# Optimization experiments

Hardware: AMD Instinct MI355X
Metric: run time of the kernel (lower is better)

The kernel has to match this reference:

```python
import jax, jax.numpy as jnp
import numpy as np

N, H, M, B = 512, 64, 1024, 256
ETA = 1.0
INIT_STD = 0.01

def setup_inputs() -> dict:
    key = jax.random.key(0)
    k1, k2, k3, k4 = jax.random.split(key, 4)
    # Binary +/-1 sequences and memory (as produced upstream in the repo)
    sequences = jnp.where(jax.random.uniform(k1, (B, N)) < 0.5, -1.0, 1.0).astype(jnp.float32)
    memory = jnp.where(jax.random.uniform(k2, (M, N)) < 0.5, -1.0, 1.0).astype(jnp.float32)
    A_logits = (INIT_STD * jax.random.normal(k3, (N, H, N))).astype(jnp.float32)
    B_logits = (INIT_STD * jax.random.normal(k4, (H, N))).astype(jnp.float32)
    return {"sequences": sequences, "memory": memory, "A_logits": A_logits, "B_logits": B_logits}

def reference(sequences, memory, A_logits, B_logits):
    # Vectorized version of DAM.train_batch's loss over positions n=1..N-1.
    n_dim = sequences.shape[1]
    # Causal mask: row for position n attends to indices i < n. Rows n=1..N-1.
    ns = jnp.arange(1, n_dim)[:, None, None]            # (N-1,1,1)
    idx = jnp.arange(n_dim)[None, None, :]              # (1,1,N)
    mask = idx < ns                                      # (N-1,1,N)
    neg_inf = jnp.asarray(-jnp.inf, A_logits.dtype)
    A = jax.nn.softmax(jnp.where(mask, A_logits[1:], neg_inf), axis=-1)  # (N-1,H,N), zeros outside mask
    Bn = jax.nn.softmax(B_logits, axis=-1)               # (H,N)
    phi_mu = jnp.einsum('hn,mn->mh', Bn, memory)         # (M,H) memory keys
    hat_phi = jnp.einsum('bi,nhi->bnh', sequences, A)    # (B,N-1,H) queries for every position at once
    score = ETA * jnp.einsum('bnh,mh->bnm', hat_phi, phi_mu)  # (B,N-1,M)
    pi = jax.nn.softmax(score, axis=-1)                  # retrieval distribution over memories
    plus = (memory[:, 1:] > 0).astype(pi.dtype)          # (M,N-1): memory bit at position n is +1
    prob = jnp.einsum('bnm,mn->bn', pi, plus)            # P(next bit = +1)
    prob = jnp.clip(prob, 1e-6, 1.0 - 1e-6)
    target = (sequences[:, 1:] > 0).astype(prob.dtype)
    bce = -(target * jnp.log(prob) + (1.0 - target) * jnp.log1p(-prob))
    # mean over batch per position, summed over positions, / (N-1) == global mean
    return jnp.mean(bce)
```

## Files before the change

### kernel.cpp

```cpp
#include <hip/hip_runtime.h>
#include <stdint.h>

#define NPOS 512
#define NH   64
#define NM   1024
#define NB   256
#define NM1  511

typedef __attribute__((ext_vector_type(8)))  short bf16x8;
typedef __attribute__((ext_vector_type(16))) float f32x16;
typedef __attribute__((ext_vector_type(4)))  float f32x4;
typedef __attribute__((ext_vector_type(4)))  int   i32x4;

#if __has_builtin(__builtin_amdgcn_exp2f)
#define EXP2F(x) __builtin_amdgcn_exp2f(x)
#else
#define EXP2F(x) __expf((x) * 0.69314718055994531f)
#endif

__device__ __forceinline__ unsigned short f2bf(float x) {
    unsigned u = __float_as_uint(x);
    u = (u + 0x7FFFu + ((u >> 16) & 1u)) >> 16;
    return (unsigned short)u;
}
__device__ __forceinline__ int pack2(unsigned short a, unsigned short b) {
    return (int)a | ((int)b << 16);
}


__global__ __launch_bounds__(256, 4)
void kAE_prep(const float* __restrict__ seq, const float* __restrict__ Bl,
              const float* __restrict__ mem, const float* __restrict__ Al,
              unsigned short* __restrict__ seq_bf, float* __restrict__ BnT,
              float* __restrict__ plusT, unsigned short* __restrict__ Ew,
              float* __restrict__ Zb, float* __restrict__ out) {
    const int bid = blockIdx.x, t = threadIdx.x;
    if (bid < 128) {
        if (bid == 0 && t == 0) out[0] = 0.f;
        int idx = (bid * 256 + t) * 4;
        f32x4 v = *(const f32x4*)(seq + idx);
        int2 o;
        o.x = pack2(f2bf(v.x), f2bf(v.y));
        o.y = pack2(f2bf(v.z), f2bf(v.w));
        *(int2*)(seq_bf + idx) = o;
    } else if (bid < 144) {
        const int h = (bid - 128) * 4 + (t >> 6), l = t & 63;
        float v[8]; float mx = -1e30f;
#pragma unroll
        for (int j = 0; j < 8; j++) { v[j] = Bl[h * NPOS + l + 64 * j]; mx = fmaxf(mx, v[j]); }
#pragma unroll
        for (int o = 32; o; o >>= 1) mx = fmaxf(mx, __shfl_xor(mx, o));
        float s = 0.f;
#pragma unroll
        for (int j = 0; j < 8; j++) { v[j] = __expf(v[j] - mx); s += v[j]; }
#pragma unroll
        for (int o = 32; o; o >>= 1) s += __shfl_xor(s, o);
        float r = 1.0f / s;
#pragma unroll
        for (int j = 0; j < 8; j++) BnT[(l + 64 * j) * NH + h] = v[j] * r;
    } else if (bid < 272) {
        __shared__ float sT[64][65];
        const int bb = bid - 144;
        const int mt = bb >> 3, nt = bb & 7;
        const int rr = t >> 2, cc = t & 3;
        const float* src = mem + (size_t)(mt * 64 + rr) * NPOS + nt * 64 + cc * 16;
#pragma unroll
        for (int j = 0; j < 4; j++) {
            f32x4 v = *(const f32x4*)(src + j * 4);
            sT[rr][cc * 16 + j * 4 + 0] = (v.x > 0.f) ? 1.f : 0.f;
            sT[rr][cc * 16 + j * 4 + 1] = (v.y > 0.f) ? 1.f : 0.f;
            sT[rr][cc * 16 + j * 4 + 2] = (v.z > 0.f) ? 1.f : 0.f;
            sT[rr][cc * 16 + j * 4 + 3] = (v.w > 0.f) ? 1.f : 0.f;
        }
        __syncthreads();
        float* dst = plusT + (size_t)(nt * 64 + rr) * NM + mt * 64 + cc * 16;
#pragma unroll
        for (int j = 0; j < 4; j++) {
            f32x4 o;
            o.x = sT[cc * 16 + j * 4 + 0][rr];
            o.y = sT[cc * 16 + j * 4 + 1][rr];
            o.z = sT[cc * 16 + j * 4 + 2][rr];
            o.w = sT[cc * 16 + j * 4 + 3][rr];
            *(f32x4*)(dst + j * 4) = o;
        }
    } else {
        const int n = bid - 271;
        const int h = t >> 2, j = t & 3;
        const int lim = ((n + 63) >> 6) * 64;
        const float* Ar = Al + ((size_t)n * NH + h) * NPOS;
        unsigned short* Er = Ew + (size_t)(n - 1) * 32768 + h * 64;
        float zp = 0.f;
#pragma unroll 4
        for (int g = 0; g < 16; g++) {
            const int i0 = g * 32 + j * 8;
            if (g * 32 >= lim) break;
            f32x4 v0 = *(const f32x4*)(Ar + i0);
            f32x4 v1 = *(const f32x4*)(Ar + i0 + 4);
            float e0 = (i0 + 0 < n) ? __expf(v0.x) : 0.f;
            float e1 = (i0 + 1 < n) ? __expf(v0.y) : 0.f;
            float e2 = (i0 + 2 < n) ? __expf(v0.z) : 0.f;
            float e3 = (i0 + 3 < n) ? __expf(v0.w) : 0.f;
            float e4 = (i0 + 4 < n) ? __expf(v1.x) : 0.f;
            float e5 = (i0 + 5 < n) ? __expf(v1.y) : 0.f;
            float e6 = (i0 + 6 < n) ? __expf(v1.z) : 0.f;
            float e7 = (i0 + 7 < n) ? __expf(v1.w) : 0.f;
            zp += ((e0 + e1) + (e2 + e3)) + ((e4 + e5) + (e6 + e7));
            i32x4 w;
            w.x = pack2(f2bf(e0), f2bf(e1));
            w.y = pack2(f2bf(e2), f2bf(e3));
            w.z = pack2(f2bf(e4), f2bf(e5));
            w.w = pack2(f2bf(e6), f2bf(e7));
            *(i32x4*)(Er + (i0 >> 6) * 4096 + (i0 & 63)) = w;
        }
        zp += __shfl_xor(zp, 1);
        zp += __shfl_xor(zp, 2);
        if (j == 0) Zb[(n - 1) * 64 + h] = zp;
    }
}

__device__ __forceinline__ void p2_load(bf16x8 (&p)[4], const unsigned short* __restrict__ phimu,
                                        int tile, int r, int half) {
#pragma unroll
    for (int kq = 0; kq < 4; kq++)
        p[kq] = *(const bf16x8*)(phimu + (size_t)(tile * 32 + r) * NH + kq * 16 + half * 8);
}
__device__ __forceinline__ void p2_mfma(const bf16x8 (&p)[4], const bf16x8 (&q0)[4], const bf16x8 (&q1)[4],
                                        const f32x16& z, f32x16& a0, f32x16& a1) {
    a0 = __builtin_amdgcn_mfma_f32_32x32x16_bf16(p[0], q0[0], z, 0, 0, 0);
    a1 = __builtin_amdgcn_mfma_f32_32x32x16_bf16(p[0], q1[0], z, 0, 0, 0);
#pragma unroll
    for (int kq = 1; kq < 4; kq++) {
        a0 = __builtin_amdgcn_mfma_f32_32x32x16_bf16(p[kq], q0[kq], a0, 0, 0, 0);
        a1 = __builtin_amdgcn_mfma_f32_32x32x16_bf16(p[kq], q1[kq], a1, 0, 0, 0);
    }
}
__device__ __forceinline__ void p2_expsum(const f32x16& a0, const f32x16& a1, const float* s_plus,
                                          int mb, int half,
                                          f32x4& den0, f32x4& num0, f32x4& den1, f32x4& num1) {
#pragma unroll
    for (int g = 0; g < 4; g++) {
        f32x4 pv = *(const f32x4*)(s_plus + mb + 4 * half + 8 * g);
        f32x4 e0, e1;
#pragma unroll
        for (int j = 0; j < 4; j++) {
            e0[j] = EXP2F(a0[4 * g + j]);
            e1[j] = EXP2F(a1[4 * g + j]);
        }
        den0 += e0; num0 += e0 * pv;
        den1 += e1; num1 += e1 * pv;
    }
}

__global__ __launch_bounds__(256, 2)
void k23_fusedE(const unsigned short* __restrict__ Ew, const float* __restrict__ Zb,
                const unsigned short* __restrict__ seq_bf,
                const unsigned short* __restrict__ phimu, const float* __restrict__ plusT,
                const float* __restrict__ seq, float* __restrict__ out) {
    __shared__ __align__(16) unsigned short e_lds[2][64 * 72];
    __shared__ __align__(16) unsigned short q_lds[256 * 72];
    __shared__ float s_plus[NM];
    __shared__ float w_lds[4];

    const int t = threadIdx.x;
    const int c = blockIdx.x >> 1;
    const int n = (blockIdx.x & 1) ? (1 + c) : (NM1 - c);
    const int ksteps = (n + 63) >> 6;
    const int wv = t >> 6, lane = t & 63, half = lane >> 5, r = lane & 31;

    *(f32x4*)(s_plus + t * 4) = *(const f32x4*)(plusT + (size_t)n * NM + t * 4);
    const float Zr0 = Zb[(n - 1) * 64 + r];
    const float Zr1 = Zb[(n - 1) * 64 + 32 + r];

    const unsigned short* Eb = Ew + (size_t)(n - 1) * 32768;
    const int eh = t >> 2, ec = (t & 3) * 16;
    const unsigned short* s0 = seq_bf + (size_t)(wv * 64 + r) * NPOS;
    const unsigned short* s1 = seq_bf + (size_t)(wv * 64 + 32 + r) * NPOS;

    f32x16 acc00, acc01, acc10, acc11;
#pragma unroll
    for (int i = 0; i < 16; i++) { acc00[i] = 0.f; acc01[i] = 0.f; acc10[i] = 0.f; acc11[i] = 0.f; }

    bf16x8 er0, er1, sc0[4], sc1[4], sn0[4], sn1[4];
    er0 = *(const bf16x8*)(Eb + eh * 64 + ec);
    er1 = *(const bf16x8*)(Eb + eh * 64 + ec + 8);
#pragma unroll
    for (int kq = 0; kq < 4; kq++) {
        sc0[kq] = *(const bf16x8*)(s0 + kq * 16 + half * 8);
        sc1[kq] = *(const bf16x8*)(s1 + kq * 16 + half * 8);
    }

    for (int kk = 0; kk < ksteps; kk++) {
        {
            unsigned short* ep = (unsigned short*)e_lds[kk & 1] + eh * 72 + ec;
            *(bf16x8*)(ep)     = er0;
            *(bf16x8*)(ep + 8) = er1;
        }
        if (kk + 1 < ksteps) {
            const unsigned short* nb = Eb + (kk + 1) * 4096 + eh * 64 + ec;
            er0 = *(const bf16x8*)(nb);
            er1 = *(const bf16x8*)(nb + 8);
            const int k0 = (kk + 1) * 64;
#pragma unroll
            for (int kq = 0; kq < 4; kq++) {
                sn0[kq] = *(const bf16x8*)(s0 + k0 + kq * 16 + half * 8);
                sn1[kq] = *(const bf16x8*)(s1 + k0 + kq * 16 + half * 8);
            }
        }
        asm volatile("s_waitcnt lgkmcnt(0)" ::: "memory");
        __builtin_amdgcn_s_barrier();
        asm volatile("" ::: "memory");
        {
            const unsigned short* sB0 = (const unsigned short*)e_lds[kk & 1] + r * 72;
            const unsigned short* sB1 = sB0 + 32 * 72;
#pragma unroll
            for (int kq = 0; kq < 4; kq++) {
                const int ko = kq * 16 + half * 8;
                bf16x8 B0 = *(const bf16x8*)(sB0 + ko);
                bf16x8 B1 = *(const bf16x8*)(sB1 + ko);
                acc00 = __builtin_amdgcn_mfma_f32_32x32x16_bf16(sc0[kq], B0, acc00, 0, 0, 0);
                acc01 = __builtin_amdgcn_mfma_f32_32x32x16_bf16(sc0[kq], B1, acc01, 0, 0, 0);
                acc10 = __builtin_amdgcn_mfma_f32_32x32x16_bf16(sc1[kq], B0, acc10, 0, 0, 0);
                acc11 = __builtin_amdgcn_mfma_f32_32x32x16_bf16(sc1[kq], B1, acc11, 0, 0, 0);
            }
        }
        if (kk + 1 < ksteps) {
#pragma unroll
            for (int kq = 0; kq < 4; kq++) { sc0[kq] = sn0[kq]; sc1[kq] = sn1[kq]; }
        }
    }
    {
        float rz0 = 1.0f / Zr0;
        float rz1 = 1.0f / Zr1;
#pragma unroll
        for (int reg = 0; reg < 16; reg++) {
            int row = (reg & 3) + 8 * (reg >> 2) + 4 * half;
            q_lds[(wv * 64 + row) * 72 + r]            = f2bf(acc00[reg] * rz0);
            q_lds[(wv * 64 + row) * 72 + 32 + r]       = f2bf(acc01[reg] * rz1);
            q_lds[(wv * 64 + 32 + row) * 72 + r]       = f2bf(acc10[reg] * rz0);
            q_lds[(wv * 64 + 32 + row) * 72 + 32 + r]  = f2bf(acc11[reg] * rz1);
        }
    }

    bf16x8 p[4], pn[4];
    p2_load(p, phimu, 0, r, half);
    bf16x8 q0[4], q1[4];
#pragma unroll
    for (int kq = 0; kq < 4; kq++) {
        q0[kq] = *(const bf16x8*)(q_lds + (wv * 64 + r) * 72 + kq * 16 + half * 8);
        q1[kq] = *(const bf16x8*)(q_lds + (wv * 64 + 32 + r) * 72 + kq * 16 + half * 8);
    }
    f32x16 zacc;
#pragma unroll
    for (int i = 0; i < 16; i++) zacc[i] = 0.f;

    f32x4 den0 = {0.f,0.f,0.f,0.f}, num0 = {0.f,0.f,0.f,0.f};
    f32x4 den1 = {0.f,0.f,0.f,0.f}, num1 = {0.f,0.f,0.f,0.f};
    f32x16 a0, a1;

    for (int it = 0; it < 32; ++it) {
        if (it < 31) p2_load(pn, phimu, it + 1, r, half);
        p2_mfma(p, q0, q1, zacc, a0, a1);
        p2_expsum(a0, a1, s_plus, it * 32, half, den0, num0, den1, num1);
        if (it < 31) {
#pragma unroll
            for (int kq = 0; kq < 4; kq++) p[kq] = pn[kq];
        }
    }

    float d0 = (den0[0] + den0[1]) + (den0[2] + den0[3]);
    float nu0 = (num0[0] + num0[1]) + (num0[2] + num0[3]);
    float d1 = (den1[0] + den1[1]) + (den1[2] + den1[3]);
    float nu1 = (num1[0] + num1[1]) + (num1[2] + num1[3]);
    d0 += __shfl_xor(d0, 32); nu0 += __shfl_xor(nu0, 32);
    d1 += __shfl_xor(d1, 32); nu1 += __shfl_xor(nu1, 32);

    float* dsum = (float*)e_lds;
    float* nsum = dsum + 256;
    if (half == 0) {
        dsum[wv * 64 + r]      = d0; nsum[wv * 64 + r]      = nu0;
        dsum[wv * 64 + 32 + r] = d1; nsum[wv * 64 + 32 + r] = nu1;
    }
    __syncthreads();
    {
        float dd = dsum[t], nn = nsum[t];
        float p2 = nn / dd;
        p2 = fminf(fmaxf(p2, 1e-6f), 1.0f - 1e-6f);
        float tg = seq[(size_t)t * NPOS + n];
        float bce = (tg > 0.f) ? -logf(p2) : -logf(1.0f - p2);
#pragma unroll
        for (int o = 32; o; o >>= 1) bce += __shfl_xor(bce, o);
        if (lane == 0) w_lds[wv] = bce;
    }
    __syncthreads();
    if (t == 0)
        atomicAdd(out, (w_lds[0] + w_lds[1] + w_lds[2] + w_lds[3]) * (1.0f / 130816.0f));
}


__global__ __launch_bounds__(256, 4)
void kA_prep(const float* __restrict__ seq, const float* __restrict__ Bl,
             const float* __restrict__ mem,
             unsigned short* __restrict__ seq_bf, float* __restrict__ BnT,
             float* __restrict__ plusT, float* __restrict__ out) {
    const int bid = blockIdx.x, t = threadIdx.x;
    if (bid < 128) {
        if (bid == 0 && t == 0) out[0] = 0.f;
        int idx = (bid * 256 + t) * 4;
        f32x4 v = *(const f32x4*)(seq + idx);
        int2 o;
        o.x = pack2(f2bf(v.x), f2bf(v.y));
        o.y = pack2(f2bf(v.z), f2bf(v.w));
        *(int2*)(seq_bf + idx) = o;
    } else if (bid < 144) {
        const int h = (bid - 128) * 4 + (t >> 6), l = t & 63;
        float v[8]; float mx = -1e30f;
#pragma unroll
        for (int j = 0; j < 8; j++) { v[j] = Bl[h * NPOS + l + 64 * j]; mx = fmaxf(mx, v[j]); }
#pragma unroll
        for (int o = 32; o; o >>= 1) mx = fmaxf(mx, __shfl_xor(mx, o));
        float s = 0.f;
#pragma unroll
        for (int j = 0; j < 8; j++) { v[j] = __expf(v[j] - mx); s += v[j]; }
#pragma unroll
        for (int o = 32; o; o >>= 1) s += __shfl_xor(s, o);
        float r = 1.0f / s;
#pragma unroll
        for (int j = 0; j < 8; j++) BnT[(l + 64 * j) * NH + h] = v[j] * r;
    } else {
        __shared__ float sT[64][65];
        const int bb = bid - 144;
        const int mt = bb >> 3, nt = bb & 7;
        const int rr = t >> 2, cc = t & 3;
        const float* src = mem + (size_t)(mt * 64 + rr) * NPOS + nt * 64 + cc * 16;
#pragma unroll
        for (int j = 0; j < 4; j++) {
            f32x4 v = *(const f32x4*)(src + j * 4);
            sT[rr][cc * 16 + j * 4 + 0] = (v.x > 0.f) ? 1.f : 0.f;
            sT[rr][cc * 16 + j * 4 + 1] = (v.y > 0.f) ? 1.f : 0.f;
            sT[rr][cc * 16 + j * 4 + 2] = (v.z > 0.f) ? 1.f : 0.f;
            sT[rr][cc * 16 + j * 4 + 3] = (v.w > 0.f) ? 1.f : 0.f;
        }
        __syncthreads();
        float* dst = plusT + (size_t)(nt * 64 + rr) * NM + mt * 64 + cc * 16;
#pragma unroll
        for (int j = 0; j < 4; j++) {
            f32x4 o;
            o.x = sT[cc * 16 + j * 4 + 0][rr];
            o.y = sT[cc * 16 + j * 4 + 1][rr];
            o.z = sT[cc * 16 + j * 4 + 2][rr];
            o.w = sT[cc * 16 + j * 4 + 3][rr];
            *(f32x4*)(dst + j * 4) = o;
        }
    }
}

__global__ __launch_bounds__(256, 2)
void k23_fused0(const float* __restrict__ Al, const unsigned short* __restrict__ seq_bf,
                const unsigned short* __restrict__ phimu, const float* __restrict__ plusT,
                const float* __restrict__ seq, float* __restrict__ out) {
    __shared__ __align__(16) unsigned short s_lds[256 * 72];
    __shared__ __align__(16) unsigned short e_lds[64 * 72];
    __shared__ float z_lds[64];
    __shared__ float s_plus[NM];

    const int t = threadIdx.x;
    const int n = NM1 - (int)blockIdx.x;
    const int ksteps = (n + 63) >> 6;
    const int wv = t >> 6, lane = t & 63, half = lane >> 5, r = lane & 31;

    if (t < 64) z_lds[t] = 0.f;
    *(f32x4*)(s_plus + t * 4) = *(const f32x4*)(plusT + n * NM + t * 4);

    const int eh = t >> 2, ei = (t & 3) * 16;
    const float* arow = Al + ((size_t)n * NH + eh) * NPOS + ei;
    const unsigned short* srcS = seq_bf + (size_t)t * NPOS;

    f32x16 acc00, acc01, acc10, acc11;
#pragma unroll
    for (int i = 0; i < 16; i++) { acc00[i] = 0.f; acc01[i] = 0.f; acc10[i] = 0.f; acc11[i] = 0.f; }

    f32x4 ea[4]; i32x4 sa[8];
#pragma unroll
    for (int g = 0; g < 4; g++) ea[g] = *(const f32x4*)(arow + g * 4);
#pragma unroll
    for (int c = 0; c < 8; c++) sa[c] = *(const i32x4*)(srcS + c * 8);
    __syncthreads();

    for (int kk = 0; kk < ksteps; kk++) {
        const int k0 = kk * 64;
        {
            float zp = 0.f;
            unsigned short* ep = e_lds + eh * 72 + ei;
#pragma unroll
            for (int g = 0; g < 4; g++) {
                int i0 = k0 + ei + g * 4;
                float e0 = (i0 + 0 < n) ? __expf(ea[g].x) : 0.f;
                float e1 = (i0 + 1 < n) ? __expf(ea[g].y) : 0.f;
                float e2 = (i0 + 2 < n) ? __expf(ea[g].z) : 0.f;
                float e3 = (i0 + 3 < n) ? __expf(ea[g].w) : 0.f;
                zp += (e0 + e1) + (e2 + e3);
                int2 o; o.x = pack2(f2bf(e0), f2bf(e1)); o.y = pack2(f2bf(e2), f2bf(e3));
                *(int2*)(ep + g * 4) = o;
            }
            zp += __shfl_xor(zp, 1);
            zp += __shfl_xor(zp, 2);
            if ((t & 3) == 0) z_lds[eh] += zp;
        }
        {
            unsigned short* dp = s_lds + t * 72;
#pragma unroll
            for (int c = 0; c < 8; c++) *(i32x4*)(dp + c * 8) = sa[c];
        }
        __syncthreads();
        if (kk + 1 < ksteps) {
#pragma unroll
            for (int g = 0; g < 4; g++) ea[g] = *(const f32x4*)(arow + k0 + 64 + g * 4);
#pragma unroll
            for (int c = 0; c < 8; c++) sa[c] = *(const i32x4*)(srcS + k0 + 64 + c * 8);
        }
        {
            const unsigned short* sA0 = s_lds + (wv * 64 + r) * 72;
            const unsigned short* sA1 = sA0 + 32 * 72;
            const unsigned short* sB0 = e_lds + r * 72;
            const unsigned short* sB1 = sB0 + 32 * 72;
#pragma unroll
            for (int kq = 0; kq < 4; kq++) {
                const int ko = kq * 16 + half * 8;
                bf16x8 A0 = *(const bf16x8*)(sA0 + ko);
                bf16x8 A1 = *(const bf16x8*)(sA1 + ko);
                bf16x8 B0 = *(const bf16x8*)(sB0 + ko);
                bf16x8 B1 = *(const bf16x8*)(sB1 + ko);
                acc00 = __builtin_amdgcn_mfma_f32_32x32x16_bf16(A0, B0, acc00, 0, 0, 0);
                acc01 = __builtin_amdgcn_mfma_f32_32x32x16_bf16(A0, B1, acc01, 0, 0, 0);
                acc10 = __builtin_amdgcn_mfma_f32_32x32x16_bf16(A1, B0, acc10, 0, 0, 0);
                acc11 = __builtin_amdgcn_mfma_f32_32x32x16_bf16(A1, B1, acc11, 0, 0, 0);
            }
        }
        __syncthreads();
    }
    {
        float rz0 = 1.0f / z_lds[r];
        float rz1 = 1.0f / z_lds[32 + r];
#pragma unroll
        for (int reg = 0; reg < 16; reg++) {
            int row = (reg & 3) + 8 * (reg >> 2) + 4 * half;
            s_lds[(wv * 64 + row) * 72 + r]            = f2bf(acc00[reg] * rz0);
            s_lds[(wv * 64 + row) * 72 + 32 + r]       = f2bf(acc01[reg] * rz1);
            s_lds[(wv * 64 + 32 + row) * 72 + r]       = f2bf(acc10[reg] * rz0);
            s_lds[(wv * 64 + 32 + row) * 72 + 32 + r]  = f2bf(acc11[reg] * rz1);
        }
    }
    __syncthreads();

    bf16x8 p[4];
#pragma unroll
    for (int kq = 0; kq < 4; kq++)
        p[kq] = *(const bf16x8*)(phimu + (r) * NH + kq * 16 + half * 8);
    bf16x8 q[2][4];
#pragma unroll
    for (int bs = 0; bs < 2; bs++)
#pragma unroll
        for (int kq = 0; kq < 4; kq++)
            q[bs][kq] = *(const bf16x8*)(s_lds + (wv * 64 + bs * 32 + r) * 72 + kq * 16 + half * 8);

    f32x4 den0 = {0.f,0.f,0.f,0.f}, num0 = {0.f,0.f,0.f,0.f};
    f32x4 den1 = {0.f,0.f,0.f,0.f}, num1 = {0.f,0.f,0.f,0.f};

    for (int it = 0; it < 32; ++it) {
        bf16x8 pn[4];
        if (it < 31) {
#pragma unroll
            for (int kq = 0; kq < 4; kq++)
                pn[kq] = *(const bf16x8*)(phimu + ((it + 1) * 32 + r) * NH + kq * 16 + half * 8);
        }
        f32x16 a0, a1;
#pragma unroll
        for (int i = 0; i < 16; i++) { a0[i] = 0.f; a1[i] = 0.f; }
#pragma unroll
        for (int kq = 0; kq < 4; kq++) {
            a0 = __builtin_amdgcn_mfma_f32_32x32x16_bf16(p[kq], q[0][kq], a0, 0, 0, 0);
            a1 = __builtin_amdgcn_mfma_f32_32x32x16_bf16(p[kq], q[1][kq], a1, 0, 0, 0);
        }
        const int mb = it * 32;
        f32x4 pv[4];
#pragma unroll
        for (int g = 0; g < 4; g++) pv[g] = *(const f32x4*)(s_plus + mb + 4 * half + 8 * g);
#pragma unroll
        for (int g = 0; g < 4; g++) {
            f32x4 e0, e1;
#pragma unroll
            for (int j = 0; j < 4; j++) {
                e0[j] = EXP2F(a0[4 * g + j]);
                e1[j] = EXP2F(a1[4 * g + j]);
            }
            den0 += e0; num0 += e0 * pv[g];
            den1 += e1; num1 += e1 * pv[g];
        }
        if (it < 31) {
#pragma unroll
            for (int kq = 0; kq < 4; kq++) p[kq] = pn[kq];
        }
    }
    float d0 = (den0[0] + den0[1]) + (den0[2] + den0[3]);
    float nu0 = (num0[0] + num0[1]) + (num0[2] + num0[3]);
    float d1 = (den1[0] + den1[1]) + (den1[2] + den1[3]);
    float nu1 = (num1[0] + num1[1]) + (num1[2] + num1[3]);
    d0 += __shfl_xor(d0, 32); nu0 += __shfl_xor(nu0, 32);
    d1 += __shfl_xor(d1, 32); nu1 += __shfl_xor(nu1, 32);

    float* dsum = (float*)e_lds;
    float* nsum = dsum + 256;
    if (half == 0) {
        dsum[wv * 64 + r]      = d0; nsum[wv * 64 + r]      = nu0;
        dsum[wv * 64 + 32 + r] = d1; nsum[wv * 64 + 32 + r] = nu1;
    }
    __syncthreads();
    {
        float dd = dsum[t], nn = nsum[t];
        float p2 = nn / dd;
        p2 = fminf(fmaxf(p2, 1e-6f), 1.0f - 1e-6f);
        float tg = seq[(size_t)t * NPOS + n];
        float bce = (tg > 0.f) ? -logf(p2) : -logf(1.0f - p2);
#pragma unroll
        for (int o = 32; o; o >>= 1) bce += __shfl_xor(bce, o);
        if (lane == 0) z_lds[wv] = bce;
    }
    __syncthreads();
    if (t == 0)
        atomicAdd(out, (z_lds[0] + z_lds[1] + z_lds[2] + z_lds[3]) * (1.0f / 130816.0f));
}

__global__ __launch_bounds__(256, 4)
void k1b_phimu(const float* __restrict__ BnT, const float* __restrict__ mem,
               unsigned short* __restrict__ phimu) {
    const int m0 = blockIdx.x * 2, t = threadIdx.x;
    __shared__ float mrow[2][NPOS];
    __shared__ float part[2][256];
    {
        int row = t >> 7, c = (t & 127) * 4;
        *(f32x4*)(&mrow[row][c]) = *(const f32x4*)(mem + (size_t)(m0 + row) * NPOS + c);
    }
    __syncthreads();
    const int h = t & 63, seg = t >> 6;
    float a[2] = {0.f, 0.f};
    float b2[2] = {0.f, 0.f};
    const float* bp = BnT + seg * 128 * NH + h;
#pragma unroll 8
    for (int nn = 0; nn < 128; nn += 2) {
        float x0 = bp[nn * NH], x1 = bp[(nn + 1) * NH];
#pragma unroll
        for (int row = 0; row < 2; row++) {
            a[row]  = fmaf(x0, mrow[row][seg * 128 + nn], a[row]);
            b2[row] = fmaf(x1, mrow[row][seg * 128 + nn + 1], b2[row]);
        }
    }
#pragma unroll
    for (int row = 0; row < 2; row++) part[row][t] = a[row] + b2[row];
    __syncthreads();
    if (t < 64) {
#pragma unroll
        for (int row = 0; row < 2; row++) {
            float s = (part[row][t] + part[row][t + 64]) + (part[row][t + 128] + part[row][t + 192]);
            phimu[(m0 + row) * NH + t] = f2bf(s * 1.4426950408889634f);
        }
    }
}

extern "C" void kernel_launch(void* const* d_in, const int* in_sizes, int n_in,
                              void* d_out, int out_size, void* d_ws, size_t ws_size,
                              hipStream_t stream) {
    const float* seq = (const float*)d_in[0];
    const float* mem = (const float*)d_in[1];
    const float* Al  = (const float*)d_in[2];
    const float* Bl  = (const float*)d_in[3];

    char* ws = (char*)d_ws;
    unsigned short* seq_bf = (unsigned short*)(ws + 0);
    float*          BnT    = (float*)(ws + 262144);
    unsigned short* phimu  = (unsigned short*)(ws + 393216);
    float*          plusT  = (float*)(ws + 524288);
    float*          Zb     = (float*)(ws + 2621440);
    unsigned short* Ew     = (unsigned short*)(ws + 2752512);
    float*          outp   = (float*)d_out;

    const size_t WS_NEEDED_E = 2752512 + (size_t)NM1 * 32768 * sizeof(unsigned short);

    if (ws_size >= WS_NEEDED_E) {
        kAE_prep<<<783, 256, 0, stream>>>(seq, Bl, mem, Al, seq_bf, BnT, plusT, Ew, Zb, outp);
        k1b_phimu<<<512, 256, 0, stream>>>(BnT, mem, phimu);
        k23_fusedE<<<511, 256, 0, stream>>>(Ew, Zb, seq_bf, phimu, plusT, seq, outp);
    } else {
        kA_prep<<<272, 256, 0, stream>>>(seq, Bl, mem, seq_bf, BnT, plusT, outp);
        k1b_phimu<<<512, 256, 0, stream>>>(BnT, mem, phimu);
        k23_fused0<<<511, 256, 0, stream>>>(Al, seq_bf, phimu, plusT, seq, outp);
    }
}
```

Measured before the change: 158.9 us.

## Split prep into per-slab blocks and halve batch per fused block

The A-softmax prep stage now launches one block per (position, 64-wide k-slab) over a packed triangular layout, so only the needed slabs are exponentiated and stored, and per-slab partial normalizers are written separately and summed later. The fused score kernel splits the batch into two halves per position, launching twice as many blocks with half the accumulators, one LDS buffer reused for E and Q, and a higher occupancy bound. This aims to spread the imbalanced triangular work more evenly across CUs and raise occupancy, at the cost of reading the E slabs twice and extra block-scheduling overhead.

```diff
diff --git a/kernel.cpp b/kernel.cpp
--- a/kernel.cpp
+++ b/kernel.cpp
@@ -26,6 +26,10 @@
 __device__ __forceinline__ int pack2(unsigned short a, unsigned short b) {
     return (int)a | ((int)b << 16);
 }
+__device__ __forceinline__ int slab_base(int n) {
+    int g = (n + 63) >> 6;
+    return 32 * (g - 1) * g + (n - 1 - (g - 1) * 64) * g;
+}
 
 
 __global__ __launch_bounds__(256, 4)
@@ -33,7 +37,7 @@
               const float* __restrict__ mem, const float* __restrict__ Al,
               unsigned short* __restrict__ seq_bf, float* __restrict__ BnT,
               float* __restrict__ plusT, unsigned short* __restrict__ Ew,
-              float* __restrict__ Zb, float* __restrict__ out) {
+              float* __restrict__ Zpart, float* __restrict__ out) {
     const int bid = blockIdx.x, t = threadIdx.x;
     if (bid < 128) {
         if (bid == 0 && t == 0) out[0] = 0.f;
@@ -84,37 +88,97 @@
             *(f32x4*)(dst + j * 4) = o;
         }
     } else {
-        const int n = bid - 271;
+        const int sid = bid - 272;
+        int g, Cp;
+        if      (sid < 64)   { g = 1; Cp = 0;    }
+        else if (sid < 192)  { g = 2; Cp = 64;   }
+        else if (sid < 384)  { g = 3; Cp = 192;  }
+        else if (sid < 640)  { g = 4; Cp = 384;  }
+        else if (sid < 960)  { g = 5; Cp = 640;  }
+        else if (sid < 1344) { g = 6; Cp = 960;  }
+        else if (sid < 1792) { g = 7; Cp = 1344; }
+        else                 { g = 8; Cp = 1792; }
+        const int off = sid - Cp;
+        const int nIdx = off / g;
+        const int kk = off - nIdx * g;
+        const int n = (g - 1) * 64 + 1 + nIdx;
+        const int sbase = 32 * (g - 1) * g + nIdx * g;
+
         const int h = t >> 2, j = t & 3;
-        const int lim = ((n + 63) >> 6) * 64;
-        const float* Ar = Al + ((size_t)n * NH + h) * NPOS;
-        unsigned short* Er = Ew + (size_t)(n - 1) * 32768 + h * 64;
+        const int i0 = kk * 64 + j * 16;
+        const float* Ar = Al + ((size_t)n * NH + h) * NPOS + i0;
+        unsigned short* Er = Ew + (size_t)(sbase + kk) * 4096 + h * 64 + j * 16;
+
+        f32x4 v0 = *(const f32x4*)(Ar + 0);
+        f32x4 v1 = *(const f32x4*)(Ar + 4);
+        f32x4 v2 = *(const f32x4*)(Ar + 8);
+        f32x4 v3 = *(const f32x4*)(Ar + 12);
+        float e[16];
+        e[0]  = (i0 + 0  < n) ? __expf(v0.x) : 0.f;
+        e[1]  = (i0 + 1  < n) ? __expf(v0.y) : 0.f;
+        e[2]  = (i0 + 2  < n) ? __expf(v0.z) : 0.f;
+        e[3]  = (i0 + 3  < n) ? __expf(v0.w) : 0.f;
+        e[4]  = (i0 + 4  < n) ? __expf(v1.x) : 0.f;
+        e[5]  = (i0 + 5  < n) ? __expf(v1.y) : 0.f;
+        e[6]  = (i0 + 6  < n) ? __expf(v1.z) : 0.f;
+        e[7]  = (i0 + 7  < n) ? __expf(v1.w) : 0.f;
+        e[8]  = (i0 + 8  < n) ? __expf(v2.x) : 0.f;
+        e[9]  = (i0 + 9  < n) ? __expf(v2.y) : 0.f;
+        e[10] = (i0 + 10 < n) ? __expf(v2.z) : 0.f;
+        e[11] = (i0 + 11 < n) ? __expf(v2.w) : 0.f;
+        e[12] = (i0 + 12 < n) ? __expf(v3.x) : 0.f;
+        e[13] = (i0 + 13 < n) ? __expf(v3.y) : 0.f;
+        e[14] = (i0 + 14 < n) ? __expf(v3.z) : 0.f;
+        e[15] = (i0 + 15 < n) ? __expf(v3.w) : 0.f;
         float zp = 0.f;
-#pragma unroll 4
-        for (int g = 0; g < 16; g++) {
-            const int i0 = g * 32 + j * 8;
-            if (g * 32 >= lim) break;
-            f32x4 v0 = *(const f32x4*)(Ar + i0);
-            f32x4 v1 = *(const f32x4*)(Ar + i0 + 4);
-            float e0 = (i0 + 0 < n) ? __expf(v0.x) : 0.f;
-            float e1 = (i0 + 1 < n) ? __expf(v0.y) : 0.f;
-            float e2 = (i0 + 2 < n) ? __expf(v0.z) : 0.f;
-            float e3 = (i0 + 3 < n) ? __expf(v0.w) : 0.f;
-            float e4 = (i0 + 4 < n) ? __expf(v1.x) : 0.f;
-            float e5 = (i0 + 5 < n) ? __expf(v1.y) : 0.f;
-            float e6 = (i0 + 6 < n) ? __expf(v1.z) : 0.f;
-            float e7 = (i0 + 7 < n) ? __expf(v1.w) : 0.f;
-            zp += ((e0 + e1) + (e2 + e3)) + ((e4 + e5) + (e6 + e7));
-            i32x4 w;
-            w.x = pack2(f2bf(e0), f2bf(e1));
-            w.y = pack2(f2bf(e2), f2bf(e3));
-            w.z = pack2(f2bf(e4), f2bf(e5));
-            w.w = pack2(f2bf(e6), f2bf(e7));
-            *(i32x4*)(Er + (i0 >> 6) * 4096 + (i0 & 63)) = w;
-        }
+#pragma unroll
+        for (int q = 0; q < 16; q++) zp += e[q];
+        i32x4 w0, w1;
+        w0.x = pack2(f2bf(e[0]),  f2bf(e[1]));  w0.y = pack2(f2bf(e[2]),  f2bf(e[3]));
+        w0.z = pack2(f2bf(e[4]),  f2bf(e[5]));  w0.w = pack2(f2bf(e[6]),  f2bf(e[7]));
+        w1.x = pack2(f2bf(e[8]),  f2bf(e[9]));  w1.y = pack2(f2bf(e[10]), f2bf(e[11]));
+        w1.z = pack2(f2bf(e[12]), f2bf(e[13])); w1.w = pack2(f2bf(e[14]), f2bf(e[15]));
+        *(i32x4*)(Er)     = w0;
+        *(i32x4*)(Er + 8) = w1;
         zp += __shfl_xor(zp, 1);
         zp += __shfl_xor(zp, 2);
-        if (j == 0) Zb[(n - 1) * 64 + h] = zp;
+        if (j == 0) Zpart[((size_t)(n - 1) * 8 + kk) * 64 + h] = zp;
+    }
+}
+
+__global__ __launch_bounds__(256, 4)
+void k1b_phimu(const float* __restrict__ BnT, const float* __restrict__ mem,
+               unsigned short* __restrict__ phimu) {
+    const int m0 = blockIdx.x * 2, t = threadIdx.x;
+    __shared__ float mrow[2][NPOS];
+    __shared__ float part[2][256];
+    {
+        int row = t >> 7, c = (t & 127) * 4;
+        *(f32x4*)(&mrow[row][c]) = *(const f32x4*)(mem + (size_t)(m0 + row) * NPOS + c);
+    }
+    __syncthreads();
+    const int h = t & 63, seg = t >> 6;
+    float a[2] = {0.f, 0.f};
+    float b2[2] = {0.f, 0.f};
+    const float* bp = BnT + seg * 128 * NH + h;
+#pragma unroll 8
+    for (int nn = 0; nn < 128; nn += 2) {
+        float x0 = bp[nn * NH], x1 = bp[(nn + 1) * NH];
+#pragma unroll
+        for (int row = 0; row < 2; row++) {
+            a[row]  = fmaf(x0, mrow[row][seg * 128 + nn], a[row]);
+            b2[row] = fmaf(x1, mrow[row][seg * 128 + nn + 1], b2[row]);
+        }
+    }
+#pragma unroll
+    for (int row = 0; row < 2; row++) part[row][t] = a[row] + b2[row];
+    __syncthreads();
+    if (t < 64) {
+#pragma unroll
+        for (int row = 0; row < 2; row++) {
+            float s = (part[row][t] + part[row][t + 64]) + (part[row][t + 128] + part[row][t + 192]);
+            phimu[(m0 + row) * NH + t] = f2bf(s * 1.4426950408889634f);
+        }
     }
 }
 
@@ -124,74 +188,51 @@
     for (int kq = 0; kq < 4; kq++)
         p[kq] = *(const bf16x8*)(phimu + (size_t)(tile * 32 + r) * NH + kq * 16 + half * 8);
 }
-__device__ __forceinline__ void p2_mfma(const bf16x8 (&p)[4], const bf16x8 (&q0)[4], const bf16x8 (&q1)[4],
-                                        const f32x16& z, f32x16& a0, f32x16& a1) {
-    a0 = __builtin_amdgcn_mfma_f32_32x32x16_bf16(p[0], q0[0], z, 0, 0, 0);
-    a1 = __builtin_amdgcn_mfma_f32_32x32x16_bf16(p[0], q1[0], z, 0, 0, 0);
-#pragma unroll
-    for (int kq = 1; kq < 4; kq++) {
-        a0 = __builtin_amdgcn_mfma_f32_32x32x16_bf16(p[kq], q0[kq], a0, 0, 0, 0);
-        a1 = __builtin_amdgcn_mfma_f32_32x32x16_bf16(p[kq], q1[kq], a1, 0, 0, 0);
-    }
-}
-__device__ __forceinline__ void p2_expsum(const f32x16& a0, const f32x16& a1, const float* s_plus,
-                                          int mb, int half,
-                                          f32x4& den0, f32x4& num0, f32x4& den1, f32x4& num1) {
-#pragma unroll
-    for (int g = 0; g < 4; g++) {
-        f32x4 pv = *(const f32x4*)(s_plus + mb + 4 * half + 8 * g);
-        f32x4 e0, e1;
-#pragma unroll
-        for (int j = 0; j < 4; j++) {
-            e0[j] = EXP2F(a0[4 * g + j]);
-            e1[j] = EXP2F(a1[4 * g + j]);
-        }
-        den0 += e0; num0 += e0 * pv;
-        den1 += e1; num1 += e1 * pv;
-    }
-}
-
-__global__ __launch_bounds__(256, 2)
-void k23_fusedE(const unsigned short* __restrict__ Ew, const float* __restrict__ Zb,
+
+__global__ __launch_bounds__(256, 4)
+void k23_fusedE(const unsigned short* __restrict__ Ew, const float* __restrict__ Zpart,
                 const unsigned short* __restrict__ seq_bf,
                 const unsigned short* __restrict__ phimu, const float* __restrict__ plusT,
                 const float* __restrict__ seq, float* __restrict__ out) {
-    __shared__ __align__(16) unsigned short e_lds[2][64 * 72];
-    __shared__ __align__(16) unsigned short q_lds[256 * 72];
+    __shared__ __align__(16) unsigned short u_lds[9216];
     __shared__ float s_plus[NM];
+    __shared__ float dn_lds[256];
     __shared__ float w_lds[4];
 
     const int t = threadIdx.x;
-    const int c = blockIdx.x >> 1;
-    const int n = (blockIdx.x & 1) ? (1 + c) : (NM1 - c);
+    const int u = blockIdx.x >> 1, bh = blockIdx.x & 1;
+    const int n = (u & 1) ? (1 + (u >> 1)) : (NM1 - (u >> 1));
+    const int boff = bh << 7;
     const int ksteps = (n + 63) >> 6;
     const int wv = t >> 6, lane = t & 63, half = lane >> 5, r = lane & 31;
 
     *(f32x4*)(s_plus + t * 4) = *(const f32x4*)(plusT + (size_t)n * NM + t * 4);
-    const float Zr0 = Zb[(n - 1) * 64 + r];
-    const float Zr1 = Zb[(n - 1) * 64 + 32 + r];
-
-    const unsigned short* Eb = Ew + (size_t)(n - 1) * 32768;
+    float Zr0 = 0.f, Zr1 = 0.f;
+    for (int kk = 0; kk < ksteps; kk++) {
+        const float* zp = Zpart + ((size_t)(n - 1) * 8 + kk) * 64;
+        Zr0 += zp[r];
+        Zr1 += zp[32 + r];
+    }
+
+    const unsigned short* Eb = Ew + (size_t)slab_base(n) * 4096;
     const int eh = t >> 2, ec = (t & 3) * 16;
-    const unsigned short* s0 = seq_bf + (size_t)(wv * 64 + r) * NPOS;
-    const unsigned short* s1 = seq_bf + (size_t)(wv * 64 + 32 + r) * NPOS;
-
-    f32x16 acc00, acc01, acc10, acc11;
-#pragma unroll
-    for (int i = 0; i < 16; i++) { acc00[i] = 0.f; acc01[i] = 0.f; acc10[i] = 0.f; acc11[i] = 0.f; }
-
-    bf16x8 er0, er1, sc0[4], sc1[4], sn0[4], sn1[4];
+    const unsigned short* s0 = seq_bf + (size_t)(boff + wv * 32 + r) * NPOS;
+
+    f32x16 acc0, acc1;
+#pragma unroll
+    for (int i = 0; i < 16; i++) { acc0[i] = 0.f; acc1[i] = 0.f; }
+
+    bf16x8 er0, er1, sc0[4], sn0[4];
     er0 = *(const bf16x8*)(Eb + eh * 64 + ec);
     er1 = *(const bf16x8*)(Eb + eh * 64 + ec + 8);
 #pragma unroll
-    for (int kq = 0; kq < 4; kq++) {
+    for (int kq = 0; kq < 4; kq++)
         sc0[kq] = *(const bf16x8*)(s0 + kq * 16 + half * 8);
-        sc1[kq] = *(const bf16x8*)(s1 + kq * 16 + half * 8);
-    }
 
     for (int kk = 0; kk < ksteps; kk++) {
+        unsigned short* ebuf = u_lds + (kk & 1) * 4608;
         {
-            unsigned short* ep = (unsigned short*)e_lds[kk & 1] + eh * 72 + ec;
+            unsigned short* ep = ebuf + eh * 72 + ec;
             *(bf16x8*)(ep)     = er0;
             *(bf16x8*)(ep + 8) = er1;
         }
@@ -201,96 +242,92 @@
             er1 = *(const bf16x8*)(nb + 8);
             const int k0 = (kk + 1) * 64;
 #pragma unroll
-            for (int kq = 0; kq < 4; kq++) {
+            for (int kq = 0; kq < 4; kq++)
                 sn0[kq] = *(const bf16x8*)(s0 + k0 + kq * 16 + half * 8);
-                sn1[kq] = *(const bf16x8*)(s1 + k0 + kq * 16 + half * 8);
-            }
         }
         asm volatile("s_waitcnt lgkmcnt(0)" ::: "memory");
         __builtin_amdgcn_s_barrier();
         asm volatile("" ::: "memory");
         {
-            const unsigned short* sB0 = (const unsigned short*)e_lds[kk & 1] + r * 72;
+            const unsigned short* sB0 = ebuf + r * 72;
             const unsigned short* sB1 = sB0 + 32 * 72;
 #pragma unroll
             for (int kq = 0; kq < 4; kq++) {
                 const int ko = kq * 16 + half * 8;
                 bf16x8 B0 = *(const bf16x8*)(sB0 + ko);
                 bf16x8 B1 = *(const bf16x8*)(sB1 + ko);
-                acc00 = __builtin_amdgcn_mfma_f32_32x32x16_bf16(sc0[kq], B0, acc00, 0, 0, 0);
-                acc01 = __builtin_amdgcn_mfma_f32_32x32x16_bf16(sc0[kq], B1, acc01, 0, 0, 0);
-                acc10 = __builtin_amdgcn_mfma_f32_32x32x16_bf16(sc1[kq], B0, acc10, 0, 0, 0);
-                acc11 = __builtin_amdgcn_mfma_f32_32x32x16_bf16(sc1[kq], B1, acc11, 0, 0, 0);
+                acc0 = __builtin_amdgcn_mfma_f32_32x32x16_bf16(sc0[kq], B0, acc0, 0, 0, 0);
+                acc1 = __builtin_amdgcn_mfma_f32_32x32x16_bf16(sc0[kq], B1, acc1, 0, 0, 0);
             }
         }
         if (kk + 1 < ksteps) {
 #pragma unroll
-            for (int kq = 0; kq < 4; kq++) { sc0[kq] = sn0[kq]; sc1[kq] = sn1[kq]; }
-        }
-    }
+            for (int kq = 0; kq < 4; kq++) sc0[kq] = sn0[kq];
+        }
+    }
+    __syncthreads();
     {
         float rz0 = 1.0f / Zr0;
         float rz1 = 1.0f / Zr1;
 #pragma unroll
         for (int reg = 0; reg < 16; reg++) {
             int row = (reg & 3) + 8 * (reg >> 2) + 4 * half;
-            q_lds[(wv * 64 + row) * 72 + r]            = f2bf(acc00[reg] * rz0);
-            q_lds[(wv * 64 + row) * 72 + 32 + r]       = f2bf(acc01[reg] * rz1);
-            q_lds[(wv * 64 + 32 + row) * 72 + r]       = f2bf(acc10[reg] * rz0);
-            q_lds[(wv * 64 + 32 + row) * 72 + 32 + r]  = f2bf(acc11[reg] * rz1);
+            u_lds[(wv * 32 + row) * 72 + r]      = f2bf(acc0[reg] * rz0);
+            u_lds[(wv * 32 + row) * 72 + 32 + r] = f2bf(acc1[reg] * rz1);
         }
     }
 
     bf16x8 p[4], pn[4];
     p2_load(p, phimu, 0, r, half);
-    bf16x8 q0[4], q1[4];
-#pragma unroll
-    for (int kq = 0; kq < 4; kq++) {
-        q0[kq] = *(const bf16x8*)(q_lds + (wv * 64 + r) * 72 + kq * 16 + half * 8);
-        q1[kq] = *(const bf16x8*)(q_lds + (wv * 64 + 32 + r) * 72 + kq * 16 + half * 8);
-    }
+    bf16x8 q0[4];
+#pragma unroll
+    for (int kq = 0; kq < 4; kq++)
+        q0[kq] = *(const bf16x8*)(u_lds + (wv * 32 + r) * 72 + kq * 16 + half * 8);
     f32x16 zacc;
 #pragma unroll
     for (int i = 0; i < 16; i++) zacc[i] = 0.f;
 
-    f32x4 den0 = {0.f,0.f,0.f,0.f}, num0 = {0.f,0.f,0.f,0.f};
-    f32x4 den1 = {0.f,0.f,0.f,0.f}, num1 = {0.f,0.f,0.f,0.f};
-    f32x16 a0, a1;
+    f32x4 den = {0.f,0.f,0.f,0.f}, num = {0.f,0.f,0.f,0.f};
+    f32x16 a0;
 
     for (int it = 0; it < 32; ++it) {
         if (it < 31) p2_load(pn, phimu, it + 1, r, half);
-        p2_mfma(p, q0, q1, zacc, a0, a1);
-        p2_expsum(a0, a1, s_plus, it * 32, half, den0, num0, den1, num1);
+        a0 = __builtin_amdgcn_mfma_f32_32x32x16_bf16(p[0], q0[0], zacc, 0, 0, 0);
+#pragma unroll
+        for (int kq = 1; kq < 4; kq++)
+            a0 = __builtin_amdgcn_mfma_f32_32x32x16_bf16(p[kq], q0[kq], a0, 0, 0, 0);
+        const int mb = it * 32;
+#pragma unroll
+        for (int g2 = 0; g2 < 4; g2++) {
+            f32x4 pv = *(const f32x4*)(s_plus + mb + 4 * half + 8 * g2);
+            f32x4 e;
+#pragma unroll
+            for (int j = 0; j < 4; j++) e[j] = EXP2F(a0[4 * g2 + j]);
+            den += e; num += e * pv;
+        }
         if (it < 31) {
 #pragma unroll
             for (int kq = 0; kq < 4; kq++) p[kq] = pn[kq];
         }
     }
 
-    float d0 = (den0[0] + den0[1]) + (den0[2] + den0[3]);
-    float nu0 = (num0[0] + num0[1]) + (num0[2] + num0[3]);
-    float d1 = (den1[0] + den1[1]) + (den1[2] + den1[3]);
-    float nu1 = (num1[0] + num1[1]) + (num1[2] + num1[3]);
-    d0 += __shfl_xor(d0, 32); nu0 += __shfl_xor(nu0, 32);
-    d1 += __shfl_xor(d1, 32); nu1 += __shfl_xor(nu1, 32);
-
-    float* dsum = (float*)e_lds;
-    float* nsum = dsum + 256;
-    if (half == 0) {
-        dsum[wv * 64 + r]      = d0; nsum[wv * 64 + r]      = nu0;
-        dsum[wv * 64 + 32 + r] = d1; nsum[wv * 64 + 32 + r] = nu1;
-    }
-    __syncthreads();
-    {
-        float dd = dsum[t], nn = nsum[t];
-        float p2 = nn / dd;
+    float d  = (den[0] + den[1]) + (den[2] + den[3]);
+    float nu = (num[0] + num[1]) + (num[2] + num[3]);
+    d += __shfl_xor(d, 32); nu += __shfl_xor(nu, 32);
+
+    if (half == 0) { dn_lds[wv * 32 + r] = d; dn_lds[128 + wv * 32 + r] = nu; }
+    __syncthreads();
+    float bce = 0.f;
+    if (t < 128) {
+        float dd = dn_lds[t], nn2 = dn_lds[128 + t];
+        float p2 = nn2 / dd;
         p2 = fminf(fmaxf(p2, 1e-6f), 1.0f - 1e-6f);
-        float tg = seq[(size_t)t * NPOS + n];
-        float bce = (tg > 0.f) ? -logf(p2) : -logf(1.0f - p2);
-#pragma unroll
-        for (int o = 32; o; o >>= 1) bce += __shfl_xor(bce, o);
-        if (lane == 0) w_lds[wv] = bce;
-    }
+        float tg = seq[(size_t)(boff + t) * NPOS + n];
+        bce = (tg > 0.f) ? -logf(p2) : -logf(1.0f - p2);
+    }
+#pragma unroll
+    for (int o = 32; o; o >>= 1) bce += __shfl_xor(bce, o);
+    if (lane == 0) w_lds[wv] = bce;
     __syncthreads();
     if (t == 0)
         atomicAdd(out, (w_lds[0] + w_lds[1] + w_lds[2] + w_lds[3]) * (1.0f / 130816.0f));
@@ -530,42 +567,6 @@
         atomicAdd(out, (z_lds[0] + z_lds[1] + z_lds[2] + z_lds[3]) * (1.0f / 130816.0f));
 }
 
-__global__ __launch_bounds__(256, 4)
-void k1b_phimu(const float* __restrict__ BnT, const float* __restrict__ mem,
-               unsigned short* __restrict__ phimu) {
-    const int m0 = blockIdx.x * 2, t = threadIdx.x;
-    __shared__ float mrow[2][NPOS];
-    __shared__ float part[2][256];
-    {
-        int row = t >> 7, c = (t & 127) * 4;
-        *(f32x4*)(&mrow[row][c]) = *(const f32x4*)(mem + (size_t)(m0 + row) * NPOS + c);
-    }
-    __syncthreads();
-    const int h = t & 63, seg = t >> 6;
-    float a[2] = {0.f, 0.f};
-    float b2[2] = {0.f, 0.f};
-    const float* bp = BnT + seg * 128 * NH + h;
-#pragma unroll 8
-    for (int nn = 0; nn < 128; nn += 2) {
-        float x0 = bp[nn * NH], x1 = bp[(nn + 1) * NH];
-#pragma unroll
-        for (int row = 0; row < 2; row++) {
-            a[row]  = fmaf(x0, mrow[row][seg * 128 + nn], a[row]);
-            b2[row] = fmaf(x1, mrow[row][seg * 128 + nn + 1], b2[row]);
-        }
-    }
-#pragma unroll
-    for (int row = 0; row < 2; row++) part[row][t] = a[row] + b2[row];
-    __syncthreads();
-    if (t < 64) {
-#pragma unroll
-        for (int row = 0; row < 2; row++) {
-            float s = (part[row][t] + part[row][t + 64]) + (part[row][t + 128] + part[row][t + 192]);
-            phimu[(m0 + row) * NH + t] = f2bf(s * 1.4426950408889634f);
-        }
-    }
-}
-
 extern "C" void kernel_launch(void* const* d_in, const int* in_sizes, int n_in,
                               void* d_out, int out_size, void* d_ws, size_t ws_size,
                               hipStream_t stream) {
@@ -579,16 +580,16 @@
     float*          BnT    = (float*)(ws + 262144);
     unsigned short* phimu  = (unsigned short*)(ws + 393216);
     float*          plusT  = (float*)(ws + 524288);
-    float*          Zb     = (float*)(ws + 2621440);
-    unsigned short* Ew     = (unsigned short*)(ws + 2752512);
+    float*          Zpart  = (float*)(ws + 2621440);
+    unsigned short* Ew     = (unsigned short*)(ws + 3670016);
     float*          outp   = (float*)d_out;
 
-    const size_t WS_NEEDED_E = 2752512 + (size_t)NM1 * 32768 * sizeof(unsigned short);
+    const size_t WS_NEEDED_E = 3670016 + (size_t)2296 * 8192;
 
     if (ws_size >= WS_NEEDED_E) {
-        kAE_prep<<<783, 256, 0, stream>>>(seq, Bl, mem, Al, seq_bf, BnT, plusT, Ew, Zb, outp);
+        kAE_prep<<<2568, 256, 0, stream>>>(seq, Bl, mem, Al, seq_bf, BnT, plusT, Ew, Zpart, outp);
         k1b_phimu<<<512, 256, 0, stream>>>(BnT, mem, phimu);
-        k23_fusedE<<<511, 256, 0, stream>>>(Ew, Zb, seq_bf, phimu, plusT, seq, outp);
+        k23_fusedE<<<1022, 256, 0, stream>>>(Ew, Zpart, seq_bf, phimu, plusT, seq, outp);
     } else {
         kA_prep<<<272, 256, 0, stream>>>(seq, Bl, mem, seq_bf, BnT, plusT, outp);
         k1b_phimu<<<512, 256, 0, stream>>>(BnT, mem, phimu);
```

After: 183.3 us. 1.15x slower.
